# Kernel optimization log

Measured on AMD Instinct MI355X. Metric: run time of the kernel, lower is better.

Reference implementation:

```python
import jax, jax.numpy as jnp
import numpy as np
import math

N_LEVELS = 16
F_PER = 2
LOG2T = 19
TABLE = 1 << LOG2T  # 524288
BASE = 16
FINEST = 512
BANDS = 10
TIME = 0.0

_B = math.exp((math.log(FINEST) - math.log(BASE)) / (N_LEVELS - 1))
_RES = [min(int(BASE * _B ** l), FINEST) for l in range(N_LEVELS)]
# primes reduced mod table size: (c*p) mod M == (c*(p mod M)) mod M, keeps products in int32 range
_PRIMES_MOD = np.array([73856093 % TABLE, 19349663 % TABLE, 83492791 % TABLE], dtype=np.int32)
_OFFSETS = np.array([[dx, dy, dz] for dx in (0, 1) for dy in (0, 1) for dz in (0, 1)], dtype=bool)  # [8,3]


def _hash_encode(x, tables):
    # x: [N,3] in [0,1]; tables: [L, 2^19, 2]
    x = jnp.clip(x, 0.0, 1.0)
    offs = jnp.asarray(_OFFSETS)[:, None, :]  # [8,1,3]
    pm = jnp.asarray(_PRIMES_MOD)
    outs = []
    for l in range(N_LEVELS):
        res = _RES[l]
        sc = x * (res - 1)                                   # [N,3]
        cf = jnp.clip(jnp.floor(sc).astype(jnp.int32), 0, res - 1)
        cc = jnp.clip(cf + 1, 0, res - 1)
        w = sc - cf.astype(sc.dtype)                         # trilinear weights [N,3]
        corner = jnp.where(offs, cc[None], cf[None])         # [8,N,3]
        h = ((corner[..., 0] * pm[0]) % TABLE
             + (corner[..., 1] * pm[1]) % TABLE
             + (corner[..., 2] * pm[2]) % TABLE) % TABLE     # [8,N]
        feats = tables[l][h]                                 # gather [8,N,2]
        cw = jnp.prod(jnp.where(offs, w[None], 1.0 - w[None]), axis=-1)  # [8,N]
        outs.append(jnp.sum(feats * cw[..., None], axis=0))  # [N,2]
    return jnp.concatenate(outs, axis=1)                     # [N,32]


def _freq_encode(freq):
    nf = (jnp.log10(jnp.clip(freq, 1e6, 1e12)) - 6.0) / 6.0  # [N,1]
    parts = []
    for i in range(BANDS):
        a = (2.0 ** i) * math.pi * nf
        parts += [jnp.sin(a), jnp.cos(a)]
    return jnp.concatenate(parts, axis=-1)                   # [N,20]


def _ln(x, g, b, eps=1e-5):
    m = jnp.mean(x, -1, keepdims=True)
    v = jnp.var(x, -1, keepdims=True)
    return (x - m) / jnp.sqrt(v + eps) * g + b


def _forward(x, frequency, tables, W0, b0, W1, b1, W2, b2, W3, b3,
             e_w1, e_b1, e_g, e_be, e_w2, e_b2,
             m_w1, m_b1, m_g, m_be, m_w2, m_b2,
             p_w1, p_b1, p_w2, p_b2,
             mat_w1, mat_b1, mat_w2, mat_b2,
             s_w1, s_b1, s_w2, s_b2):
    pe = _hash_encode(x, tables)                             # [N,32]
    fe = _freq_encode(frequency)                             # [N,20]
    feat0 = jnp.concatenate([pe, fe], axis=1)                # [N,52]
    h = jax.nn.relu(feat0 @ W0 + b0)
    h = jax.nn.relu(h @ W1 + b1)
    h = jax.nn.relu(jnp.concatenate([h, feat0], axis=1) @ W2 + b2)  # skip connection
    h = jax.nn.relu(h @ W3 + b3)
    E_amp = jnp.tanh(jax.nn.relu(_ln(h @ e_w1 + e_b1, e_g, e_be)) @ e_w2 + e_b2)
    B_amp = jnp.tanh(jax.nn.relu(_ln(h @ m_w1 + m_b1, m_g, m_be)) @ m_w2 + m_b2)
    phases = jax.nn.relu(h @ p_w1 + p_b1) @ p_w2 + p_b2      # [N,6]
    mat = jax.nn.relu(h @ mat_w1 + mat_b1) @ mat_w2 + mat_b2 # [N,3]
    src = jax.nn.relu(h @ s_w1 + s_b1) @ s_w2 + s_b2         # [N,4]
    omega = 2.0 * math.pi * frequency                        # [N,1]
    E = E_amp * jnp.cos(omega * TIME + phases[:, :3])
    B = B_amp * jnp.cos(omega * TIME + phases[:, 3:])
    eps_r = 1.0 + jax.nn.sigmoid(mat[:, 0:1]) * 10.0
    mu_r = 1.0 + jax.nn.sigmoid(mat[:, 1:2]) * 2.0
    cond = jax.nn.sigmoid(mat[:, 2:3]) * 0.01
    # pack all float outputs: E(3) B(3) eps(1) mu(1) cond(1) charge(1) current(3)
    return jnp.concatenate([E, B, eps_r, mu_r, cond, src[:, 0:1], src[:, 1:4]], axis=1)


def _lin_init(k, fan_in, fan_out):
    k1, k2 = jax.random.split(k)
    s = 1.0 / math.sqrt(fan_in)
    W = jax.random.uniform(k1, (fan_in, fan_out), jnp.float32, -s, s)
    b = jax.random.uniform(k2, (fan_out,), jnp.float32, -s, s)
    return W, b


def setup_inputs() -> dict:
    key = jax.random.key(0)
    ks = jax.random.split(key, 20)
    N = 262144
    d = {}
    d['x'] = jax.random.uniform(ks[0], (N, 3), jnp.float32)
    d['frequency'] = 10.0 ** jax.random.uniform(ks[1], (N, 1), jnp.float32, minval=6.0, maxval=12.0)
    d['tables'] = jax.random.normal(ks[2], (N_LEVELS, TABLE, F_PER), jnp.float32) * 1e-4
    layers = [('W0', 'b0', 52, 128), ('W1', 'b1', 128, 128), ('W2', 'b2', 180, 128), ('W3', 'b3', 128, 128),
              ('e_w1', 'e_b1', 128, 64), ('e_w2', 'e_b2', 64, 3),
              ('m_w1', 'm_b1', 128, 64), ('m_w2', 'm_b2', 64, 3),
              ('p_w1', 'p_b1', 128, 32), ('p_w2', 'p_b2', 32, 6),
              ('mat_w1', 'mat_b1', 128, 64), ('mat_w2', 'mat_b2', 64, 3),
              ('s_w1', 's_b1', 128, 64), ('s_w2', 's_b2', 64, 4)]
    for j, (wn, bn, fi, fo) in enumerate(layers):
        W, b = _lin_init(jax.random.fold_in(ks[3], j), fi, fo)
        d[wn] = W
        d[bn] = b
    d['e_g'] = jnp.ones(64, jnp.float32)
    d['e_be'] = jnp.zeros(64, jnp.float32)
    d['m_g'] = jnp.ones(64, jnp.float32)
    d['m_be'] = jnp.zeros(64, jnp.float32)
    return d


def reference(x, frequency, tables, W0, b0, W1, b1, W2, b2, W3, b3,
              e_w1, e_b1, e_g, e_be, e_w2, e_b2,
              m_w1, m_b1, m_g, m_be, m_w2, m_b2,
              p_w1, p_b1, p_w2, p_b2,
              mat_w1, mat_b1, mat_w2, mat_b2,
              s_w1, s_b1, s_w2, s_b2):
    return _forward(x, frequency, tables, W0, b0, W1, b1, W2, b2, W3, b3,
                    e_w1, e_b1, e_g, e_be, e_w2, e_b2,
                    m_w1, m_b1, m_g, m_be, m_w2, m_b2,
                    p_w1, p_b1, p_w2, p_b2,
                    mat_w1, mat_b1, mat_w2, mat_b2,
                    s_w1, s_b1, s_w2, s_b2)
```

## Files before the change

kernel.cpp:

```cpp
#include <hip/hip_runtime.h>
#include <math.h>

#define TMASK 524287
#define PM0 455773
#define PM1 475295
#define PM2 130999

typedef __attribute__((ext_vector_type(8))) short bf16x8;
typedef __attribute__((ext_vector_type(4))) float f32x4;

#define OFF_W0   0
#define OFF_W1   8192
#define OFF_W2   24576
#define OFF_W3   49152
#define OFF_E    65536
#define OFF_P    81920
#define OFF_MAT  86016
#define OFF_S    94208
#define OFF_BD   102400
#define WT_TOTAL 102400
#define WT_ALLOC 111616

#define WS_TAB8_OFF (WT_ALLOC*2)
#define TAB8_BYTES  (16u*524288u*2u)
#define WS_FEAT_OFF (WS_TAB8_OFF + TAB8_BYTES)
#define DENSE_USHORTS 1023640
#define DENSE_BYTES   (DENSE_USHORTS*2)

#define TAB_SCALE   131072.0f
#define TAB_INV     (1.0f/131072.0f)

#define A6_H    0
#define A6_HL   8704
#define A6_FB   8704
#define LDS6_TOTAL 17408

struct Params {
  const float* x; const float* freq; const float* tables;
  const float* b0; const float* b1; const float* b2; const float* b3;
  const float* e_b1; const float* e_w2; const float* e_b2; const float* e_g; const float* e_be;
  const float* m_b1; const float* m_w2; const float* m_b2; const float* m_g; const float* m_be;
  const float* p_b1; const float* p_w2; const float* p_b2;
  const float* mat_b1; const float* mat_w2; const float* mat_b2;
  const float* s_b1; const float* s_w2; const float* s_b2;
  const short* wt;
  const unsigned* feat;
  const unsigned short* dense;
  float* out;
  int N;
  int res[16];
};

struct HashParams {
  const float* x; const unsigned short* tab8; unsigned* feat; int N; int res[16];
};
struct DensePrepParams { const unsigned short* tab8; unsigned short* dense; };
struct TabPrepParams { const float* tables; unsigned* tab8; };
struct PrepParams {
  const float* src[9];
  int end[9]; int Nsrc[9]; int Ksrc[9]; int Kpad[9];
  short* wt;
};
struct BdParams {
  const float* e; const float* m; const float* p; const float* mat; const float* s;
  short* out;
};

__device__ __forceinline__ short f2bf(float f){
  union { float f; unsigned u; } v; v.f = f;
  unsigned r = v.u + 0x7fffu + ((v.u >> 16) & 1u);
  return (short)(r >> 16);
}
__device__ __forceinline__ float bf2f(short s){
  union { unsigned u; float f; } v; v.u = ((unsigned)(unsigned short)s) << 16; return v.f;
}
__device__ __forceinline__ float sigmoid_(float v){ return 1.f/(1.f + expf(-v)); }

__global__ __launch_bounds__(256)
void prep_weights(PrepParams P)
{
  int id = blockIdx.x*256 + threadIdx.x;
  if (id >= WT_TOTAL) return;
  int r = 0, base = 0;
  #pragma unroll
  for (int i = 0; i < 9; ++i) { if (id >= P.end[i]) { r = i+1; base = P.end[i]; } }
  const int rel = id - base;
  const int kp = P.Kpad[r];
  const int n = rel / kp;
  const int k = rel - n*kp;
  float v = 0.f;
  if (k < P.Ksrc[r]) v = P.src[r][k * P.Nsrc[r] + n];
  P.wt[id] = f2bf(v);
}

__global__ __launch_bounds__(256)
void prep_bd(BdParams P)
{
  int id = blockIdx.x*256 + threadIdx.x;
  if (id >= 32*288) return;
  const int n = id / 288, k = id - n*288;
  float v = 0.f;
  if      (n < 3  && k < 64)                        v = P.e[k*3 + n];
  else if (n >= 3 && n < 6  && k >= 64  && k < 128) v = P.m[(k-64)*3 + (n-3)];
  else if (n >= 6 && n < 12 && k >= 256)            v = P.p[(k-256)*6 + (n-6)];
  else if (n >= 12&& n < 15 && k >= 128 && k < 192) v = P.mat[(k-128)*3 + (n-12)];
  else if (n >= 15&& n < 19 && k >= 192 && k < 256) v = P.s[(k-192)*4 + (n-15)];
  P.out[id] = f2bf(v);
}

__global__ __launch_bounds__(256)
void tab_prep(TabPrepParams P)
{
  const unsigned id = blockIdx.x*256 + threadIdx.x;
  if (id >= 16u*524288u/2u) return;
  const float4 v = ((const float4*)P.tables)[id];
  int q0 = (int)fminf(fmaxf(rintf(v.x*TAB_SCALE), -127.f), 127.f);
  int q1 = (int)fminf(fmaxf(rintf(v.y*TAB_SCALE), -127.f), 127.f);
  int q2 = (int)fminf(fmaxf(rintf(v.z*TAB_SCALE), -127.f), 127.f);
  int q3 = (int)fminf(fmaxf(rintf(v.w*TAB_SCALE), -127.f), 127.f);
  unsigned pack = (q0 & 255) | ((q1 & 255) << 8) | ((q2 & 255) << 16) | ((q3 & 255) << 24);
  P.tab8[id] = pack;
}

__global__ __launch_bounds__(256)
void dense_prep8(DensePrepParams P)
{
  const int id = blockIdx.x*256 + threadIdx.x;
  if (id >= DENSE_USHORTS) return;
  int l = 0, base = 0, res = 16;
  if (id >= 4096)   { l = 1; base = 4096;   res = 20; }
  if (id >= 12096)  { l = 2; base = 12096;  res = 25; }
  if (id >= 27728)  { l = 3; base = 27728;  res = 32; }
  if (id >= 60496)  { l = 4; base = 60496;  res = 40; }
  if (id >= 124496) { l = 5; base = 124496; res = 50; }
  if (id >= 249496) { l = 6; base = 249496; res = 64; }
  if (id >= 511640) { l = 7; base = 511640; res = 80; }
  const int c = id - base;
  if (c >= res*res*res) return;
  const int cz = c % res;
  const int t  = c / res;
  const int cy = t % res;
  const int cx = t / res;
  const unsigned h = (unsigned)((cx*PM0 + cy*PM1 + cz*PM2) & TMASK);
  P.dense[id] = P.tab8[((unsigned)l << 19) + h];
}

__global__ __launch_bounds__(256, 8)
void hash_encode8lv(HashParams P)
{
  const int b = blockIdx.x;
  const int unit = b % 16;
  const int strip = b / 16;
  const int l = 8 + (unit >> 1);
  const int half = unit & 1;
  const int halfN = (P.N + 1) >> 1;
  const int plA = strip*512 + threadIdx.x;
  if (plA >= halfN) return;
  const int plB = plA + 256;
  const bool vB = plB < halfN;
  int pA = half*halfN + plA;
  int pB = half*halfN + (vB ? plB : plA);
  const bool sA = pA < P.N;
  const bool sB = vB && (pB < P.N);
  if (pA >= P.N) pA = P.N - 1;
  if (pB >= P.N) pB = P.N - 1;

  const int res = P.res[l];
  const float rf = (float)(res-1);
  const unsigned short* tp = P.tab8 + ((size_t)l << 19);

  const float xA0 = fminf(fmaxf(P.x[pA*3+0], 0.f), 1.f);
  const float xA1 = fminf(fmaxf(P.x[pA*3+1], 0.f), 1.f);
  const float xA2 = fminf(fmaxf(P.x[pA*3+2], 0.f), 1.f);
  const float sA0 = xA0*rf, sA1 = xA1*rf, sA2 = xA2*rf;
  int fA0 = (int)sA0; if (fA0 > res-1) fA0 = res-1;
  int fA1 = (int)sA1; if (fA1 > res-1) fA1 = res-1;
  int fA2 = (int)sA2; if (fA2 > res-1) fA2 = res-1;
  const float wA0 = sA0 - (float)fA0;
  const float wA1 = sA1 - (float)fA1;
  const float wA2 = sA2 - (float)fA2;
  int cA0 = fA0+1; if (cA0 > res-1) cA0 = res-1;
  int cA1 = fA1+1; if (cA1 > res-1) cA1 = res-1;
  int cA2 = fA2+1; if (cA2 > res-1) cA2 = res-1;
  const int hxA0 = (fA0*PM0) & TMASK, hxA1 = (cA0*PM0) & TMASK;
  const int hyA0 = (fA1*PM1) & TMASK, hyA1 = (cA1*PM1) & TMASK;
  const int hzA0 = (fA2*PM2) & TMASK, hzA1 = (cA2*PM2) & TMASK;

  const float xB0 = fminf(fmaxf(P.x[pB*3+0], 0.f), 1.f);
  const float xB1 = fminf(fmaxf(P.x[pB*3+1], 0.f), 1.f);
  const float xB2 = fminf(fmaxf(P.x[pB*3+2], 0.f), 1.f);
  const float sB0 = xB0*rf, sB1 = xB1*rf, sB2 = xB2*rf;
  int fB0 = (int)sB0; if (fB0 > res-1) fB0 = res-1;
  int fB1 = (int)sB1; if (fB1 > res-1) fB1 = res-1;
  int fB2 = (int)sB2; if (fB2 > res-1) fB2 = res-1;
  const float wB0 = sB0 - (float)fB0;
  const float wB1 = sB1 - (float)fB1;
  const float wB2 = sB2 - (float)fB2;
  int cB0 = fB0+1; if (cB0 > res-1) cB0 = res-1;
  int cB1 = fB1+1; if (cB1 > res-1) cB1 = res-1;
  int cB2 = fB2+1; if (cB2 > res-1) cB2 = res-1;
  const int hxB0 = (fB0*PM0) & TMASK, hxB1 = (cB0*PM0) & TMASK;
  const int hyB0 = (fB1*PM1) & TMASK, hyB1 = (cB1*PM1) & TMASK;
  const int hzB0 = (fB2*PM2) & TMASK, hzB1 = (cB2*PM2) & TMASK;

  unsigned short tvA[8], tvB[8];
  #pragma unroll
  for (int cn = 0; cn < 8; ++cn) {
    const int bx = (cn>>2)&1, by = (cn>>1)&1, bz = cn&1;
    tvA[cn] = tp[((bx?hxA1:hxA0) + (by?hyA1:hyA0) + (bz?hzA1:hzA0)) & TMASK];
    tvB[cn] = tp[((bx?hxB1:hxB0) + (by?hyB1:hyB0) + (bz?hzB1:hzB0)) & TMASK];
  }

  unsigned* fl = P.feat + (size_t)(l-8)*P.N;
  {
    float a0 = 0.f, a1 = 0.f;
    #pragma unroll
    for (int cn = 0; cn < 8; ++cn) {
      const int bx = (cn>>2)&1, by = (cn>>1)&1, bz = cn&1;
      const float cw = (bx?wA0:1.f-wA0)*(by?wA1:1.f-wA1)*(bz?wA2:1.f-wA2);
      a0 = fmaf(cw, (float)(int)(signed char)(tvA[cn] & 0xff), a0);
      a1 = fmaf(cw, (float)(int)(signed char)(tvA[cn] >> 8),   a1);
    }
    a0 *= TAB_INV; a1 *= TAB_INV;
    if (sA)
      fl[pA] = (unsigned)(unsigned short)f2bf(a0)
             | ((unsigned)(unsigned short)f2bf(a1) << 16);
  }
  {
    float a0 = 0.f, a1 = 0.f;
    #pragma unroll
    for (int cn = 0; cn < 8; ++cn) {
      const int bx = (cn>>2)&1, by = (cn>>1)&1, bz = cn&1;
      const float cw = (bx?wB0:1.f-wB0)*(by?wB1:1.f-wB1)*(bz?wB2:1.f-wB2);
      a0 = fmaf(cw, (float)(int)(signed char)(tvB[cn] & 0xff), a0);
      a1 = fmaf(cw, (float)(int)(signed char)(tvB[cn] >> 8),   a1);
    }
    a0 *= TAB_INV; a1 *= TAB_INV;
    if (sB)
      fl[pB] = (unsigned)(unsigned short)f2bf(a0)
             | ((unsigned)(unsigned short)f2bf(a1) << 16);
  }
}

__device__ __forceinline__ unsigned dense_blend(
    const unsigned short* __restrict__ dp, int res,
    float xs0, float xs1, float xs2)
{
  const float rf = (float)(res-1);
  const float s0 = xs0*rf, s1 = xs1*rf, s2 = xs2*rf;
  int f0i = (int)s0; if (f0i > res-1) f0i = res-1;
  int f1i = (int)s1; if (f1i > res-1) f1i = res-1;
  int f2i = (int)s2; if (f2i > res-1) f2i = res-1;
  const float w0 = s0 - (float)f0i;
  const float w1 = s1 - (float)f1i;
  const float w2 = s2 - (float)f2i;
  int c0i = f0i+1; if (c0i > res-1) c0i = res-1;
  int c1i = f1i+1; if (c1i > res-1) c1i = res-1;
  int c2i = f2i+1; if (c2i > res-1) c2i = res-1;
  const int sx0 = f0i*res*res, sx1 = c0i*res*res;
  const int ty0 = f1i*res,     ty1 = c1i*res;
  unsigned short tv[8];
  #pragma unroll
  for (int cn = 0; cn < 8; ++cn) {
    const int bx = (cn>>2)&1, by = (cn>>1)&1, bz = cn&1;
    tv[cn] = dp[(bx?sx1:sx0) + (by?ty1:ty0) + (bz?c2i:f2i)];
  }
  float a0 = 0.f, a1 = 0.f;
  #pragma unroll
  for (int cn = 0; cn < 8; ++cn) {
    const int bx = (cn>>2)&1, by = (cn>>1)&1, bz = cn&1;
    const float cw = (bx?w0:1.f-w0)*(by?w1:1.f-w1)*(bz?w2:1.f-w2);
    a0 = fmaf(cw, (float)(int)(signed char)(tv[cn] & 0xff), a0);
    a1 = fmaf(cw, (float)(int)(signed char)(tv[cn] >> 8),   a1);
  }
  a0 *= TAB_INV; a1 *= TAB_INV;
  return (unsigned)(unsigned short)f2bf(a0)
       | ((unsigned)(unsigned short)f2bf(a1) << 16);
}

template<int NT, int KC>
__device__ __forceinline__ void gemm32(f32x4* acc0, f32x4* acc1,
    const short* A, int lda, const short* __restrict__ wt, int kpad, int kwoff,
    int n0, int q)
{
  const short* Ap0 = A + n0*lda + q*8;
  const short* Ap1 = Ap0 + 16*lda;
  const short* Bp  = wt + n0*kpad + kwoff + q*8;
  bf16x8 bc[NT], bn[NT];
  #pragma unroll
  for (int nt = 0; nt < NT; ++nt) bc[nt] = *(const bf16x8*)(Bp + nt*16*kpad);
  #pragma unroll
  for (int kc = 0; kc < KC; ++kc) {
    if (kc + 1 < KC) {
      #pragma unroll
      for (int nt = 0; nt < NT; ++nt)
        bn[nt] = *(const bf16x8*)(Bp + nt*16*kpad + (kc+1)*32);
    }
    const bf16x8 a0 = *(const bf16x8*)(Ap0 + kc*32);
    const bf16x8 a1 = *(const bf16x8*)(Ap1 + kc*32);
    #pragma unroll
    for (int nt = 0; nt < NT; ++nt) {
      acc0[nt] = __builtin_amdgcn_mfma_f32_16x16x32_bf16(a0, bc[nt], acc0[nt], 0, 0, 0);
      acc1[nt] = __builtin_amdgcn_mfma_f32_16x16x32_bf16(a1, bc[nt], acc1[nt], 0, 0, 0);
    }
    #pragma unroll
    for (int nt = 0; nt < NT; ++nt) bc[nt] = bn[nt];
  }
}

template<int NT>
__device__ __forceinline__ void epi_trunk(const f32x4* acc0, const f32x4* acc1,
    const float* bv4, short* out, int ldo, int n0, int q, int coff)
{
  #pragma unroll
  for (int nt = 0; nt < NT; ++nt) {
    const float bv = bv4[nt];
    #pragma unroll
    for (int r = 0; r < 4; ++r) {
      float v0 = fmaxf(acc0[nt][r] + bv, 0.f);
      float v1 = fmaxf(acc1[nt][r] + bv, 0.f);
      out[(q*4 + r)*ldo + coff + nt*16 + n0]      = f2bf(v0);
      out[(16 + q*4 + r)*ldo + coff + nt*16 + n0] = f2bf(v1);
    }
  }
}

__global__ __launch_bounds__(128, 4)
void em_nerf6(Params P)
{
  __shared__ __align__(16) char smem[LDS6_TOTAL];
  const int tid = threadIdx.x;
  const int lane = tid & 63, wave = tid >> 6;
  short* H  = (short*)(smem + A6_H);
  short* HL = (short*)(smem + A6_HL);
  short* FB = (short*)(smem + A6_FB);
  float* R2 = (float*)(smem + A6_HL);
  const int n0 = lane & 15, q = lane >> 4;
  const int p0 = blockIdx.x*32;
  const int ntb = wave*64;

  const int pp = tid & 31;
  const int lg = tid >> 5;
  int gp = p0 + pp; if (gp >= P.N) gp = P.N - 1;

  unsigned fw2[2];
  #pragma unroll
  for (int j = 0; j < 2; ++j)
    fw2[j] = P.feat[(size_t)(lg*2 + j)*P.N + gp];

  const float xs0 = fminf(fmaxf(P.x[gp*3+0], 0.f), 1.f);
  const float xs1 = fminf(fmaxf(P.x[gp*3+1], 0.f), 1.f);
  const float xs2 = fminf(fmaxf(P.x[gp*3+2], 0.f), 1.f);

  float rb0[4], rb1[4], rb2[4], rb3[4], rbem[4], rbms[4], rg[4], rbe[4];
  {
    const float* embp = wave ? P.m_b1 : P.e_b1;
    const float* msbp = wave ? P.s_b1 : P.mat_b1;
    const float* ggp  = wave ? P.m_g  : P.e_g;
    const float* bbep = wave ? P.m_be : P.e_be;
    #pragma unroll
    for (int nt = 0; nt < 4; ++nt) {
      const int c  = ntb + nt*16 + n0;
      const int ch = nt*16 + n0;
      rb0[nt] = P.b0[c]; rb1[nt] = P.b1[c]; rb2[nt] = P.b2[c]; rb3[nt] = P.b3[c];
      rbem[nt] = embp[ch]; rbms[nt] = msbp[ch];
      rg[nt] = ggp[ch]; rbe[nt] = bbep[ch];
    }
  }
  const float rpb = P.p_b1[wave*16 + n0];
  float rc;
  if (wave == 0) {
    if      (n0 < 3)  rc = P.e_b2[n0];
    else if (n0 < 6)  rc = P.m_b2[n0-3];
    else if (n0 < 12) rc = P.p_b2[n0-6];
    else if (n0 < 15) rc = P.mat_b2[n0-12];
    else              rc = P.s_b2[0];
  } else {
    rc = (n0 < 3) ? P.s_b2[1 + n0] : 0.f;
  }

  unsigned coarse_pack;
  {
    const int lo  = (lg & 1) ? 20 : 16;
    const int hi  = (lg & 1) ? 32 : 25;
    const int res = (lg & 2) ? hi : lo;
    const unsigned dlo  = (lg & 1) ? 4096u  : 0u;
    const unsigned dhi  = (lg & 1) ? 27728u : 12096u;
    const unsigned doff = (lg & 2) ? dhi : dlo;
    coarse_pack = dense_blend(P.dense + doff, res, xs0, xs1, xs2);
  }

  unsigned mid_pack;
  {
    const int lo  = (lg & 1) ? 50 : 40;
    const int hi  = (lg & 1) ? 80 : 64;
    const int res = (lg & 2) ? hi : lo;
    const unsigned dlo  = (lg & 1) ? 124496u : 60496u;
    const unsigned dhi  = (lg & 1) ? 511640u : 249496u;
    const unsigned doff = (lg & 2) ? dhi : dlo;
    mid_pack = dense_blend(P.dense + doff, res, xs0, xs1, xs2);
  }

  {
    float fr = P.freq[gp];
    fr = fminf(fmaxf(fr, 1e6f), 1e12f);
    const float nf = (log10f(fr) - 6.f) * (1.f/6.f);
    const float a0 = 3.14159274101257324f * nf;
    #pragma clang loop unroll(disable)
    for (int i = lg; i < 10; i += 4) {
      const float a = a0 * (float)(1 << i);
      FB[pp*72 + 32 + 2*i] = f2bf(sinf(a));
      FB[pp*72 + 33 + 2*i] = f2bf(cosf(a));
    }
    if (lg == 3) {
      #pragma unroll
      for (int k = 52; k < 64; ++k) FB[pp*72 + k] = 0;
    }
  }

  *(unsigned*)&FB[pp*72 + 2*lg] = coarse_pack;
  *(unsigned*)&FB[pp*72 + 8 + 2*lg] = mid_pack;
  #pragma unroll
  for (int j = 0; j < 2; ++j)
    *(unsigned*)&FB[pp*72 + 16 + 4*lg + 2*j] = fw2[j];
  __syncthreads();

  { f32x4 a0[4] = {}, a1[4] = {};
    gemm32<4,2>(a0, a1, FB, 72, P.wt + OFF_W0 + ntb*64, 64, 0, n0, q);
    epi_trunk<4>(a0, a1, rb0, H, 136, n0, q, ntb);
    __syncthreads(); }
  { f32x4 a0[4] = {}, a1[4] = {};
    gemm32<4,4>(a0, a1, H, 136, P.wt + OFF_W1 + ntb*128, 128, 0, n0, q);
    __syncthreads();
    epi_trunk<4>(a0, a1, rb1, H, 136, n0, q, ntb);
    __syncthreads(); }
  { f32x4 a0[4] = {}, a1[4] = {};
    gemm32<4,4>(a0, a1, H, 136, P.wt + OFF_W2 + ntb*192, 192, 0, n0, q);
    gemm32<4,2>(a0, a1, FB, 72, P.wt + OFF_W2 + ntb*192, 192, 128, n0, q);
    __syncthreads();
    epi_trunk<4>(a0, a1, rb2, H, 136, n0, q, ntb);
    __syncthreads(); }
  { f32x4 a0[4] = {}, a1[4] = {};
    gemm32<4,4>(a0, a1, H, 136, P.wt + OFF_W3 + ntb*128, 128, 0, n0, q);
    __syncthreads();
    epi_trunk<4>(a0, a1, rb3, H, 136, n0, q, ntb);
    __syncthreads(); }

  { f32x4 a0[4] = {}, a1[4] = {};
    gemm32<4,4>(a0, a1, H, 136, P.wt + OFF_E + ntb*128, 128, 0, n0, q);
    #pragma unroll
    for (int nt = 0; nt < 4; ++nt) {
      const float bv = rbem[nt];
      #pragma unroll
      for (int r = 0; r < 4; ++r) { a0[nt][r] += bv; a1[nt][r] += bv; }
    }
    float mn[2][4], iv[2][4];
    #pragma unroll
    for (int s = 0; s < 2; ++s) {
      const f32x4* A_ = s ? a1 : a0;
      #pragma unroll
      for (int r = 0; r < 4; ++r) {
        float se = 0.f, qe = 0.f;
        #pragma unroll
        for (int t = 0; t < 4; ++t) { const float x = A_[t][r]; se += x; qe = fmaf(x,x,qe); }
        #pragma unroll
        for (int msk = 1; msk < 16; msk <<= 1) {
          se += __shfl_xor(se, msk, 64);
          qe += __shfl_xor(qe, msk, 64);
        }
        const float me = se*(1.f/64.f);
        mn[s][r] = me;
        iv[s][r] = 1.f / sqrtf(qe*(1.f/64.f) - me*me + 1e-5f);
      }
    }
    #pragma unroll
    for (int t = 0; t < 4; ++t) {
      const float g  = rg[t];
      const float be = rbe[t];
      const int col = ntb + t*16 + n0;
      #pragma unroll
      for (int s = 0; s < 2; ++s) {
        const f32x4* A_ = s ? a1 : a0;
        #pragma unroll
        for (int r = 0; r < 4; ++r) {
          float v = (A_[t][r] - mn[s][r])*iv[s][r]*g + be;
          v = fmaxf(v, 0.f);
          HL[(s*16 + q*4 + r)*136 + col] = f2bf(v);
        }
      }
    }
  }
  __syncthreads();

  f32x4 o0[1] = {}, o1[1] = {};
  gemm32<1,4>(o0, o1, HL, 136, P.wt + OFF_BD + wave*16*288, 288, 0, n0, q);

  { f32x4 a0[4] = {}, a1[4] = {};
    gemm32<4,4>(a0, a1, H, 136, P.wt + OFF_MAT + ntb*128, 128, 0, n0, q);
    __syncthreads();
    #pragma unroll
    for (int t = 0; t < 4; ++t) {
      const float bv = rbms[t];
      const int col = ntb + t*16 + n0;
      #pragma unroll
      for (int s = 0; s < 2; ++s) {
        const f32x4* A_ = s ? a1 : a0;
        #pragma unroll
        for (int r = 0; r < 4; ++r)
          HL[(s*16 + q*4 + r)*136 + col] = f2bf(fmaxf(A_[t][r] + bv, 0.f));
      }
    }
  }
  __syncthreads();

  gemm32<1,4>(o0, o1, HL, 136, P.wt + OFF_BD + wave*16*288, 288, 128, n0, q);

  { f32x4 a0[1] = {}, a1[1] = {};
    gemm32<1,4>(a0, a1, H, 136, P.wt + OFF_P + wave*16*128, 128, 0, n0, q);
    __syncthreads();
    const int col = wave*16 + n0;
    #pragma unroll
    for (int s = 0; s < 2; ++s) {
      const f32x4* A_ = s ? a1 : a0;
      #pragma unroll
      for (int r = 0; r < 4; ++r)
        HL[(s*16 + q*4 + r)*136 + col] = f2bf(fmaxf(A_[0][r] + rpb, 0.f));
    }
  }
  __syncthreads();

  gemm32<1,1>(o0, o1, HL, 136, P.wt + OFF_BD + wave*16*288, 288, 256, n0, q);
  __syncthreads();

  #pragma unroll
  for (int s = 0; s < 2; ++s) {
    const f32x4* O_ = s ? o1 : o0;
    #pragma unroll
    for (int r = 0; r < 4; ++r) {
      const int p = s*16 + q*4 + r;
      if (wave == 0) {
        float v0 = O_[0][r] + rc;
        if (n0 < 6) v0 = tanhf(v0);
        R2[p*20 + n0] = v0;
      } else if (n0 < 3) {
        R2[p*20 + 16 + n0] = O_[0][r] + rc;
      }
    }
  }
  __syncthreads();

  if (tid < 32) {
    const int gp2 = p0 + tid;
    if (gp2 < P.N) {
      const float* r = R2 + tid*20;
      float* o = P.out + (size_t)gp2*13;
      o[0] = r[0]*cosf(r[6]);
      o[1] = r[1]*cosf(r[7]);
      o[2] = r[2]*cosf(r[8]);
      o[3] = r[3]*cosf(r[9]);
      o[4] = r[4]*cosf(r[10]);
      o[5] = r[5]*cosf(r[11]);
      o[6] = 1.f + sigmoid_(r[12])*10.f;
      o[7] = 1.f + sigmoid_(r[13])*2.f;
      o[8] = sigmoid_(r[14])*0.01f;
      o[9]  = r[15];
      o[10] = r[16];
      o[11] = r[17];
      o[12] = r[18];
    }
  }
}

__global__ __launch_bounds__(256, 3)
void em_nerf_fallback(Params P)
{
  __shared__ __align__(16) char smem[44288];
  short* featB = (short*)smem;
  short* hA    = (short*)(smem + 9216);
  short* hB    = (short*)(smem + 9216 + 17664);
  float* headF = (float*)(smem + 9216);
  float* res2  = (float*)smem;
  __shared__ int s_res[16];

  const int tid = threadIdx.x;
  if (tid < 16) s_res[tid] = P.res[tid];
  __syncthreads();
  {
    const int p = tid & 63;
    const int g = tid >> 6;
    int gp = blockIdx.x*64 + p; if (gp >= P.N) gp = P.N - 1;
    const float xs0 = fminf(fmaxf(P.x[gp*3+0], 0.f), 1.f);
    const float xs1 = fminf(fmaxf(P.x[gp*3+1], 0.f), 1.f);
    const float xs2 = fminf(fmaxf(P.x[gp*3+2], 0.f), 1.f);
    #pragma unroll
    for (int j = 0; j < 4; ++j) {
      const int l = g*4 + j;
      const int res = s_res[l];
      const float rf = (float)(res-1);
      const float s0 = xs0*rf, s1 = xs1*rf, s2 = xs2*rf;
      int f0i = (int)s0; if (f0i > res-1) f0i = res-1;
      int f1i = (int)s1; if (f1i > res-1) f1i = res-1;
      int f2i = (int)s2; if (f2i > res-1) f2i = res-1;
      const float w0 = s0 - (float)f0i;
      const float w1 = s1 - (float)f1i;
      const float w2 = s2 - (float)f2i;
      int c0i = f0i+1; if (c0i > res-1) c0i = res-1;
      int c1i = f1i+1; if (c1i > res-1) c1i = res-1;
      int c2i = f2i+1; if (c2i > res-1) c2i = res-1;
      const int hx0 = (f0i*PM0) & TMASK, hx1 = (c0i*PM0) & TMASK;
      const int hy0 = (f1i*PM1) & TMASK, hy1 = (c1i*PM1) & TMASK;
      const int hz0 = (f2i*PM2) & TMASK, hz1 = (c2i*PM2) & TMASK;
      const float* tp = P.tables + ((size_t)l << 20);
      float a0 = 0.f, a1 = 0.f;
      #pragma unroll
      for (int cn = 0; cn < 8; ++cn) {
        const int bx = (cn>>2)&1, by = (cn>>1)&1, bz = cn&1;
        const int hh = ((bx?hx1:hx0) + (by?hy1:hy0) + (bz?hz1:hz0)) & TMASK;
        const float cw = (bx?w0:1.f-w0)*(by?w1:1.f-w1)*(bz?w2:1.f-w2);
        const float2 tv = *(const float2*)(tp + 2*hh);
        a0 = fmaf(cw, tv.x, a0);
        a1 = fmaf(cw, tv.y, a1);
      }
      featB[p*72 + 2*l]   = f2bf(a0);
      featB[p*72 + 2*l+1] = f2bf(a1);
    }
    if (g == 0) {
      float fr = P.freq[gp];
      fr = fminf(fmaxf(fr, 1e6f), 1e12f);
      const float nf = (log10f(fr) - 6.f) * (1.f/6.f);
      float a = 3.14159274101257324f * nf;
      #pragma unroll
      for (int i = 0; i < 10; ++i) {
        featB[p*72 + 32 + 2*i] = f2bf(sinf(a));
        featB[p*72 + 33 + 2*i] = f2bf(cosf(a));
        a = a * 2.f;
      }
    }
    if (g == 3) {
      #pragma unroll
      for (int k = 52; k < 64; ++k) featB[p*72 + k] = 0;
    }
  }
  __syncthreads();

  const int lane = tid & 63, wave = tid >> 6;
  const int n0 = lane & 15, q = lane >> 4;
  short* myA  = featB + wave*16*72;
  short* myH1 = hA + wave*16*136;
  short* myH2 = hB + wave*16*136;

  auto gemm1 = [&](const short* A, int lda, const short* wt, int kpad, int kwoff, int KC, f32x4* acc, int NT){
    const short* Ap = A + n0*lda + q*8;
    const short* Bp = wt + n0*kpad + kwoff + q*8;
    for (int kc = 0; kc < KC; ++kc) {
      bf16x8 a = *(const bf16x8*)(Ap + kc*32);
      for (int nt = 0; nt < NT; ++nt) {
        bf16x8 b = *(const bf16x8*)(Bp + nt*16*kpad + kc*32);
        acc[nt] = __builtin_amdgcn_mfma_f32_16x16x32_bf16(a, b, acc[nt], 0, 0, 0);
      }
    }
  };
  auto epi1 = [&](const f32x4* acc, const float* bias, short* out, int ldo, int NT, bool relu){
    for (int nt = 0; nt < NT; ++nt) {
      const float bv = bias[nt*16 + n0];
      for (int r = 0; r < 4; ++r) {
        float v = acc[nt][r] + bv;
        if (relu) v = fmaxf(v, 0.f);
        out[(q*4 + r)*ldo + nt*16 + n0] = f2bf(v);
      }
    }
  };

  { f32x4 acc[8] = {}; gemm1(myA, 72, P.wt + OFF_W0, 64, 0, 2, acc, 8);  epi1(acc, P.b0, myH1, 136, 8, true); }
  __syncthreads();
  { f32x4 acc[8] = {}; gemm1(myH1, 136, P.wt + OFF_W1, 128, 0, 4, acc, 8); epi1(acc, P.b1, myH2, 136, 8, true); }
  __syncthreads();
  { f32x4 acc[8] = {}; gemm1(myH2, 136, P.wt + OFF_W2, 192, 0, 4, acc, 8);
    gemm1(myA, 72, P.wt + OFF_W2, 192, 128, 2, acc, 8); epi1(acc, P.b2, myH1, 136, 8, true); }
  __syncthreads();
  { f32x4 acc[8] = {}; gemm1(myH1, 136, P.wt + OFF_W3, 128, 0, 4, acc, 8); epi1(acc, P.b3, myH2, 136, 8, true); }
  __syncthreads();

  float* hf = headF + wave*16*69;
  auto head1f = [&](const short* wt, const float* bias, int NT, bool relu){
    f32x4 acc[4] = {};
    gemm1(myH2, 136, wt, 128, 0, 4, acc, NT);
    for (int nt = 0; nt < NT; ++nt) {
      const float bv = bias[nt*16 + n0];
      for (int r = 0; r < 4; ++r) {
        float v = acc[nt][r] + bv;
        if (relu) v = fmaxf(v, 0.f);
        hf[(q*4 + r)*69 + nt*16 + n0] = v;
      }
    }
  };
  auto l2 = [&](int OC2, int K2, bool ln, bool th, const float* g, const float* be,
                const float* W2, const float* b2, int slot){
    __syncthreads();
    if (tid < 64) {
      const float* row = headF + tid*69;
      float mn = 0.f, iv = 1.f;
      if (ln) {
        float s = 0.f;
        for (int k = 0; k < K2; ++k) s += row[k];
        mn = s/(float)K2;
        float vv = 0.f;
        for (int k = 0; k < K2; ++k) { float d = row[k]-mn; vv = fmaf(d,d,vv); }
        iv = 1.f/sqrtf(vv/(float)K2 + 1e-5f);
      }
      for (int j = 0; j < OC2; ++j) {
        float acc = b2[j];
        for (int k = 0; k < K2; ++k) {
          float xv = row[k];
          if (ln) xv = (xv-mn)*iv*g[k] + be[k];
          xv = fmaxf(xv, 0.f);
          acc = fmaf(xv, W2[k*OC2+j], acc);
        }
        res2[tid*20 + slot + j] = th ? tanhf(acc) : acc;
      }
    }
    __syncthreads();
  };

  head1f(P.wt + OFF_E, P.e_b1, 4, false); l2(3, 64, true,  true,  P.e_g, P.e_be, P.e_w2, P.e_b2, 0);
  head1f(P.wt + OFF_E + 8192, P.m_b1, 4, false); l2(3, 64, true, true, P.m_g, P.m_be, P.m_w2, P.m_b2, 3);
  head1f(P.wt + OFF_P, P.p_b1, 2, true);  l2(6, 32, false, false, 0, 0, P.p_w2, P.p_b2, 6);
  head1f(P.wt + OFF_MAT, P.mat_b1, 4, true); l2(3, 64, false, false, 0, 0, P.mat_w2, P.mat_b2, 12);
  head1f(P.wt + OFF_S, P.s_b1, 4, true);  l2(4, 64, false, false, 0, 0, P.s_w2, P.s_b2, 15);

  if (tid < 64) {
    const int gp = blockIdx.x*64 + tid;
    if (gp < P.N) {
      const float* r = res2 + tid*20;
      float* o = P.out + (size_t)gp*13;
      o[0] = r[0]*cosf(r[6]);
      o[1] = r[1]*cosf(r[7]);
      o[2] = r[2]*cosf(r[8]);
      o[3] = r[3]*cosf(r[9]);
      o[4] = r[4]*cosf(r[10]);
      o[5] = r[5]*cosf(r[11]);
      o[6] = 1.f + sigmoid_(r[12])*10.f;
      o[7] = 1.f + sigmoid_(r[13])*2.f;
      o[8] = sigmoid_(r[14])*0.01f;
      o[9]  = r[15];
      o[10] = r[16];
      o[11] = r[17];
      o[12] = r[18];
    }
  }
}

extern "C" void kernel_launch(void* const* d_in, const int* in_sizes, int n_in,
                              void* d_out, int out_size, void* d_ws, size_t ws_size,
                              hipStream_t stream) {
  (void)n_in; (void)out_size;
  const float** in = (const float**)d_in;
  const int N = in_sizes[0] / 3;

  PrepParams PP;
  const float* srcs[9] = { in[3], in[5], in[7], in[9], in[11], in[15], in[19], in[23], in[27] };
  const int ends[9]  = { 8192, 24576, 49152, 65536, 73728, 81920, 86016, 94208, 102400 };
  const int nsrc[9]  = { 128, 128, 128, 128, 64, 64, 32, 64, 64 };
  const int ksrc[9]  = { 52, 128, 180, 128, 128, 128, 128, 128, 128 };
  const int kpad[9]  = { 64, 128, 192, 128, 128, 128, 128, 128, 128 };
  for (int i = 0; i < 9; ++i) { PP.src[i]=srcs[i]; PP.end[i]=ends[i]; PP.Nsrc[i]=nsrc[i]; PP.Ksrc[i]=ksrc[i]; PP.Kpad[i]=kpad[i]; }
  PP.wt = (short*)d_ws;
  hipLaunchKernelGGL(prep_weights, dim3((WT_TOTAL+255)/256), dim3(256), 0, stream, PP);

  BdParams BP;
  BP.e = in[13]; BP.m = in[17]; BP.p = in[21]; BP.mat = in[25]; BP.s = in[29];
  BP.out = (short*)d_ws + OFF_BD;
  hipLaunchKernelGGL(prep_bd, dim3((32*288 + 255)/256), dim3(256), 0, stream, BP);

  Params P;
  P.x = in[0]; P.freq = in[1]; P.tables = in[2];
  P.b0 = in[4]; P.b1 = in[6]; P.b2 = in[8]; P.b3 = in[10];
  P.e_b1 = in[12]; P.e_w2 = in[13]; P.e_b2 = in[14];
  P.m_b1 = in[16]; P.m_w2 = in[17]; P.m_b2 = in[18];
  P.p_b1 = in[20]; P.p_w2 = in[21]; P.p_b2 = in[22];
  P.mat_b1 = in[24]; P.mat_w2 = in[25]; P.mat_b2 = in[26];
  P.s_b1 = in[28]; P.s_w2 = in[29]; P.s_b2 = in[30];
  P.e_g = in[31]; P.e_be = in[32]; P.m_g = in[33]; P.m_be = in[34];
  P.wt = (const short*)d_ws;
  P.feat = (const unsigned*)((const char*)d_ws + WS_FEAT_OFF);
  P.out = (float*)d_out;
  P.N = N;

  const double B = exp((log(512.0) - log(16.0)) / 15.0);
  for (int l = 0; l < 16; ++l) {
    double r = 16.0 * pow(B, (double)l);
    int ri = (int)r;
    if (ri > 512) ri = 512;
    P.res[l] = ri;
  }

  const size_t feat_bytes = (size_t)N*8*4;
  const size_t need = (size_t)WS_FEAT_OFF + feat_bytes + DENSE_BYTES;

  if (ws_size >= need) {
    char* dense_base = (char*)d_ws + WS_FEAT_OFF + feat_bytes;
    P.dense = (const unsigned short*)dense_base;

    TabPrepParams TP;
    TP.tables = in[2];
    TP.tab8 = (unsigned*)((char*)d_ws + WS_TAB8_OFF);
    hipLaunchKernelGGL(tab_prep, dim3((16*524288/2 + 255)/256), dim3(256), 0, stream, TP);

    DensePrepParams DP;
    DP.tab8 = (const unsigned short*)((const char*)d_ws + WS_TAB8_OFF);
    DP.dense = (unsigned short*)dense_base;
    hipLaunchKernelGGL(dense_prep8, dim3((DENSE_USHORTS + 255)/256), dim3(256), 0, stream, DP);

    HashParams HP;
    HP.x = in[0];
    HP.tab8 = (const unsigned short*)((const char*)d_ws + WS_TAB8_OFF);
    HP.feat = (unsigned*)((char*)d_ws + WS_FEAT_OFF);
    HP.N = N;
    for (int l = 0; l < 16; ++l) HP.res[l] = P.res[l];
    const int halfN = (N + 1) >> 1;
    const int strips = (halfN + 511) / 512;
    hipLaunchKernelGGL(hash_encode8lv, dim3(strips*16), dim3(256), 0, stream, HP);

    hipLaunchKernelGGL(em_nerf6, dim3((N + 31) / 32), dim3(128), 0, stream, P);
  } else {
    P.dense = nullptr;
    hipLaunchKernelGGL(em_nerf_fallback, dim3((N + 63) / 64), dim3(256), 0, stream, P);
  }
}
```

Baseline: 471.2 us.

## Process 64 points per block using two independent LDS arenas of 32 points

Measured after the change: 499.9 us. +6.1%, slower.

```diff
diff --git a/kernel.cpp b/kernel.cpp
--- a/kernel.cpp
+++ b/kernel.cpp
@@ -33,7 +33,8 @@
 #define A6_H    0
 #define A6_HL   8704
 #define A6_FB   8704
-#define LDS6_TOTAL 17408
+#define ARENA6  17408
+#define LDS6_TOTAL (2*ARENA6)
 
 struct Params {
   const float* x; const float* freq; const float* tables;
@@ -325,23 +326,27 @@
   }
 }
 
-__global__ __launch_bounds__(128, 4)
+__global__ __launch_bounds__(256, 4)
 void em_nerf6(Params P)
 {
   __shared__ __align__(16) char smem[LDS6_TOTAL];
   const int tid = threadIdx.x;
   const int lane = tid & 63, wave = tid >> 6;
-  short* H  = (short*)(smem + A6_H);
-  short* HL = (short*)(smem + A6_HL);
-  short* FB = (short*)(smem + A6_FB);
-  float* R2 = (float*)(smem + A6_HL);
+  const int m = wave >> 1;
+  const int w = wave & 1;
+  char* arena = smem + m*ARENA6;
+  short* H  = (short*)(arena + A6_H);
+  short* HL = (short*)(arena + A6_HL);
+  float* R2 = (float*)(arena + A6_HL);
   const int n0 = lane & 15, q = lane >> 4;
-  const int p0 = blockIdx.x*32;
-  const int ntb = wave*64;
-
-  const int pp = tid & 31;
-  const int lg = tid >> 5;
-  int gp = p0 + pp; if (gp >= P.N) gp = P.N - 1;
+  const int p0 = blockIdx.x*64;
+  const int ntb = w*64;
+
+  const int pp2 = tid & 63;
+  const int lg = tid >> 6;
+  short* FBs = (short*)(smem + (pp2 >> 5)*ARENA6 + A6_FB);
+  const int prow = (pp2 & 31)*72;
+  int gp = p0 + pp2; if (gp >= P.N) gp = P.N - 1;
 
   unsigned fw2[2];
   #pragma unroll
@@ -354,10 +359,10 @@
 
   float rb0[4], rb1[4], rb2[4], rb3[4], rbem[4], rbms[4], rg[4], rbe[4];
   {
-    const float* embp = wave ? P.m_b1 : P.e_b1;
-    const float* msbp = wave ? P.s_b1 : P.mat_b1;
-    const float* ggp  = wave ? P.m_g  : P.e_g;
-    const float* bbep = wave ? P.m_be : P.e_be;
+    const float* embp = w ? P.m_b1 : P.e_b1;
+    const float* msbp = w ? P.s_b1 : P.mat_b1;
+    const float* ggp  = w ? P.m_g  : P.e_g;
+    const float* bbep = w ? P.m_be : P.e_be;
     #pragma unroll
     for (int nt = 0; nt < 4; ++nt) {
       const int c  = ntb + nt*16 + n0;
@@ -367,9 +372,9 @@
       rg[nt] = ggp[ch]; rbe[nt] = bbep[ch];
     }
   }
-  const float rpb = P.p_b1[wave*16 + n0];
+  const float rpb = P.p_b1[w*16 + n0];
   float rc;
-  if (wave == 0) {
+  if (w == 0) {
     if      (n0 < 3)  rc = P.e_b2[n0];
     else if (n0 < 6)  rc = P.m_b2[n0-3];
     else if (n0 < 12) rc = P.p_b2[n0-6];
@@ -409,21 +414,23 @@
     #pragma clang loop unroll(disable)
     for (int i = lg; i < 10; i += 4) {
       const float a = a0 * (float)(1 << i);
-      FB[pp*72 + 32 + 2*i] = f2bf(sinf(a));
-      FB[pp*72 + 33 + 2*i] = f2bf(cosf(a));
+      FBs[prow + 32 + 2*i] = f2bf(sinf(a));
+      FBs[prow + 33 + 2*i] = f2bf(cosf(a));
     }
     if (lg == 3) {
       #pragma unroll
-      for (int k = 52; k < 64; ++k) FB[pp*72 + k] = 0;
-    }
-  }
-
-  *(unsigned*)&FB[pp*72 + 2*lg] = coarse_pack;
-  *(unsigned*)&FB[pp*72 + 8 + 2*lg] = mid_pack;
+      for (int k = 52; k < 64; ++k) FBs[prow + k] = 0;
+    }
+  }
+
+  *(unsigned*)&FBs[prow + 2*lg] = coarse_pack;
+  *(unsigned*)&FBs[prow + 8 + 2*lg] = mid_pack;
   #pragma unroll
   for (int j = 0; j < 2; ++j)
-    *(unsigned*)&FB[pp*72 + 16 + 4*lg + 2*j] = fw2[j];
-  __syncthreads();
+    *(unsigned*)&FBs[prow + 16 + 4*lg + 2*j] = fw2[j];
+  __syncthreads();
+
+  short* FB = (short*)(arena + A6_FB);
 
   { f32x4 a0[4] = {}, a1[4] = {};
     gemm32<4,2>(a0, a1, FB, 72, P.wt + OFF_W0 + ntb*64, 64, 0, n0, q);
@@ -493,7 +500,7 @@
   __syncthreads();
 
   f32x4 o0[1] = {}, o1[1] = {};
-  gemm32<1,4>(o0, o1, HL, 136, P.wt + OFF_BD + wave*16*288, 288, 0, n0, q);
+  gemm32<1,4>(o0, o1, HL, 136, P.wt + OFF_BD + w*16*288, 288, 0, n0, q);
 
   { f32x4 a0[4] = {}, a1[4] = {};
     gemm32<4,4>(a0, a1, H, 136, P.wt + OFF_MAT + ntb*128, 128, 0, n0, q);
@@ -513,12 +520,12 @@
   }
   __syncthreads();
 
-  gemm32<1,4>(o0, o1, HL, 136, P.wt + OFF_BD + wave*16*288, 288, 128, n0, q);
+  gemm32<1,4>(o0, o1, HL, 136, P.wt + OFF_BD + w*16*288, 288, 128, n0, q);
 
   { f32x4 a0[1] = {}, a1[1] = {};
-    gemm32<1,4>(a0, a1, H, 136, P.wt + OFF_P + wave*16*128, 128, 0, n0, q);
+    gemm32<1,4>(a0, a1, H, 136, P.wt + OFF_P + w*16*128, 128, 0, n0, q);
     __syncthreads();
-    const int col = wave*16 + n0;
+    const int col = w*16 + n0;
     #pragma unroll
     for (int s = 0; s < 2; ++s) {
       const f32x4* A_ = s ? a1 : a0;
@@ -529,7 +536,7 @@
   }
   __syncthreads();
 
-  gemm32<1,1>(o0, o1, HL, 136, P.wt + OFF_BD + wave*16*288, 288, 256, n0, q);
+  gemm32<1,1>(o0, o1, HL, 136, P.wt + OFF_BD + w*16*288, 288, 256, n0, q);
   __syncthreads();
 
   #pragma unroll
@@ -538,7 +545,7 @@
     #pragma unroll
     for (int r = 0; r < 4; ++r) {
       const int p = s*16 + q*4 + r;
-      if (wave == 0) {
+      if (w == 0) {
         float v0 = O_[0][r] + rc;
         if (n0 < 6) v0 = tanhf(v0);
         R2[p*20 + n0] = v0;
@@ -549,10 +556,10 @@
   }
   __syncthreads();
 
-  if (tid < 32) {
+  if (tid < 64) {
     const int gp2 = p0 + tid;
     if (gp2 < P.N) {
-      const float* r = R2 + tid*20;
+      const float* r = (float*)(smem + (tid>>5)*ARENA6 + A6_HL) + (tid & 31)*20;
       float* o = P.out + (size_t)gp2*13;
       o[0] = r[0]*cosf(r[6]);
       o[1] = r[1]*cosf(r[7]);
@@ -821,7 +828,7 @@
     const int strips = (halfN + 511) / 512;
     hipLaunchKernelGGL(hash_encode8lv, dim3(strips*16), dim3(256), 0, stream, HP);
 
-    hipLaunchKernelGGL(em_nerf6, dim3((N + 31) / 32), dim3(128), 0, stream, P);
+    hipLaunchKernelGGL(em_nerf6, dim3((N + 63) / 64), dim3(256), 0, stream, P);
   } else {
     P.dense = nullptr;
     hipLaunchKernelGGL(em_nerf_fallback, dim3((N + 63) / 64), dim3(256), 0, stream, P);
```
